# Kernel tuning notes

Hardware: AMD Instinct MI355X
Metric: run time of the kernel (lower is better)

The kernel has to match this reference:

```python
import jax, jax.numpy as jnp
import numpy as np

N_NODES = 50000
N_EDGES = 1600000
IN_DIM = 128
HEADS = 2
OUT_CH = 32
NEG_SLOPE = 0.2


def setup_inputs() -> dict:
    key = jax.random.key(0)
    k1, k2, k3, k4, k5, k6 = jax.random.split(key, 6)
    x = jax.random.normal(k1, (N_NODES, IN_DIM), dtype=jnp.float32)
    # Glorot-ish scale for weights
    W = jax.random.normal(k2, (IN_DIM, HEADS * OUT_CH), dtype=jnp.float32) * (1.0 / np.sqrt(IN_DIM))
    att_src = jax.random.normal(k3, (HEADS, OUT_CH), dtype=jnp.float32) * (1.0 / np.sqrt(OUT_CH))
    att_dst = jax.random.normal(k4, (HEADS, OUT_CH), dtype=jnp.float32) * (1.0 / np.sqrt(OUT_CH))
    bias = jnp.zeros((HEADS * OUT_CH,), dtype=jnp.float32)
    edge_index = jax.random.randint(k5, (2, N_EDGES), 0, N_NODES, dtype=jnp.int32)
    return {"x": x, "W": W, "att_src": att_src, "att_dst": att_dst,
            "bias": bias, "edge_index": edge_index}


def reference(x, W, att_src, att_dst, bias, edge_index):
    N = x.shape[0]
    # ELU on input features (IntraGraphAttention.forward)
    xf = jax.nn.elu(x)
    # Shared linear projection, per-head view: [N, H, C]
    h = (xf @ W).reshape(N, HEADS, OUT_CH)
    # add_self_loops=True (PyG GATConv default)
    loops = jnp.arange(N, dtype=edge_index.dtype)
    src = jnp.concatenate([edge_index[0], loops])
    dst = jnp.concatenate([edge_index[1], loops])
    # Per-node attention halves: [N, H]
    a_src = jnp.einsum('nhc,hc->nh', h, att_src)
    a_dst = jnp.einsum('nhc,hc->nh', h, att_dst)
    # Per-edge logits with leaky relu: [E, H]
    logits = a_src[src] + a_dst[dst]
    logits = jnp.where(logits >= 0, logits, NEG_SLOPE * logits)
    # Segment softmax over incoming edges of each dst node
    seg_max = jax.ops.segment_max(logits, dst, num_segments=N)
    e = jnp.exp(logits - seg_max[dst])
    denom = jax.ops.segment_sum(e, dst, num_segments=N)
    alpha = e / (denom[dst] + 1e-16)  # [E, H]
    # Weighted scatter-aggregate of source features: [N, H, C]
    msgs = h[src] * alpha[:, :, None]
    out = jax.ops.segment_sum(msgs, dst, num_segments=N)
    # concat=True -> [N, H*C], plus bias
    return out.reshape(N, HEADS * OUT_CH) + bias
```

## Files before the change

### kernel.cpp

```cpp
#include <hip/hip_runtime.h>
#include <hip/hip_bf16.h>

#define NN 50000
#define EE 1600000

using short8 = __attribute__((ext_vector_type(8))) short;
using float4v = __attribute__((ext_vector_type(4))) float;

__device__ __forceinline__ float bflo(unsigned u) { return __uint_as_float(u << 16); }
__device__ __forceinline__ float bfhi(unsigned u) { return __uint_as_float(u & 0xffff0000u); }
__device__ __forceinline__ unsigned short f2bf(float v) {
  return __bfloat16_as_ushort(__float2bfloat16(v));
}

__global__ __launch_bounds__(256) void k_pre(
    const float* __restrict__ x, const float* __restrict__ W,
    const float* __restrict__ att_src, const float* __restrict__ att_dst,
    float2* __restrict__ a_src2, float2* __restrict__ a_dst2,
    int* __restrict__ head8, int nblocks) {
  __shared__ float wa_s[128][2], wa_d[128][2];
  int tid = threadIdx.x;
  {
    int k = tid >> 1, hh = tid & 1;
    const float* wrow = W + k * 64 + hh * 32;
    const float* as = att_src + hh * 32;
    const float* ad = att_dst + hh * 32;
    float ss = 0.f, dd = 0.f;
#pragma unroll 8
    for (int c = 0; c < 32; ++c) { float wv = wrow[c]; ss += wv * as[c]; dd += wv * ad[c]; }
    wa_s[k][hh] = ss; wa_d[k][hh] = dd;
  }
  int gsize = nblocks * 256;
  for (int i = blockIdx.x * 256 + tid; i < NN * 8; i += gsize) head8[i] = -1;
  __syncthreads();
  int w = tid >> 6, lane = tid & 63;
  int nwaves = nblocks * 4;
  for (int n = blockIdx.x * 4 + w; n < NN; n += nwaves) {
    float x0 = x[n * 128 + lane], x1 = x[n * 128 + 64 + lane];
    x0 = x0 > 0.f ? x0 : __expf(x0) - 1.f;
    x1 = x1 > 0.f ? x1 : __expf(x1) - 1.f;
    float s0 = x0 * wa_s[lane][0] + x1 * wa_s[lane + 64][0];
    float s1 = x0 * wa_s[lane][1] + x1 * wa_s[lane + 64][1];
    float d0 = x0 * wa_d[lane][0] + x1 * wa_d[lane + 64][0];
    float d1 = x0 * wa_d[lane][1] + x1 * wa_d[lane + 64][1];
#pragma unroll
    for (int o = 32; o > 0; o >>= 1) {
      s0 += __shfl_xor(s0, o); s1 += __shfl_xor(s1, o);
      d0 += __shfl_xor(d0, o); d1 += __shfl_xor(d1, o);
    }
    if (lane == 0) { a_src2[n] = make_float2(s0, s1); a_dst2[n] = make_float2(d0, d1); }
  }
}

__global__ __launch_bounds__(256) void k_projm(
    const float* __restrict__ x, const float* __restrict__ W,
    unsigned* __restrict__ h2u) {
  __shared__ unsigned short Wt[64 * 136];
  __shared__ unsigned short xs[64 * 136];
  int tid = threadIdx.x;
  int row0 = blockIdx.x * 64;
  for (int i = tid; i < 8192; i += 256) {
    int k = i >> 6, n = i & 63;
    Wt[n * 136 + k] = f2bf(W[i]);
  }
  for (int i = tid; i < 4096; i += 256) {
    int r = i >> 6, k2 = (i & 63) * 2;
    int row = row0 + r;
    float v0 = 0.f, v1 = 0.f;
    if (row < NN) { float2 xv = *(const float2*)&x[row * 128 + k2]; v0 = xv.x; v1 = xv.y; }
    v0 = v0 > 0.f ? v0 : __expf(v0) - 1.f;
    v1 = v1 > 0.f ? v1 : __expf(v1) - 1.f;
    *(unsigned*)&xs[r * 136 + k2] = (unsigned)f2bf(v0) | ((unsigned)f2bf(v1) << 16);
  }
  __syncthreads();
  int w = tid >> 6, lane = tid & 63;
  int m = lane & 15, quad = lane >> 4;
  float4v acc[4] = {{0,0,0,0},{0,0,0,0},{0,0,0,0},{0,0,0,0}};
#pragma unroll
  for (int ks = 0; ks < 4; ++ks) {
    int koff = quad * 8 + ks * 32;
    short8 af = *(const short8*)&xs[(w * 16 + m) * 136 + koff];
#pragma unroll
    for (int nt = 0; nt < 4; ++nt) {
      short8 bf = *(const short8*)&Wt[(nt * 16 + m) * 136 + koff];
      acc[nt] = __builtin_amdgcn_mfma_f32_16x16x32_bf16(af, bf, acc[nt], 0, 0, 0);
    }
  }
#pragma unroll
  for (int nt = 0; nt < 4; ++nt) {
#pragma unroll
    for (int reg = 0; reg < 4; ++reg) {
      float v = acc[nt][reg];
      float vhi = __shfl_xor(v, 1);
      int row = row0 + w * 16 + quad * 4 + reg;
      if (!(m & 1) && row < NN) {
        h2u[row * 32 + nt * 8 + (m >> 1)] =
            (unsigned)f2bf(v) | ((unsigned)f2bf(vhi) << 16);
      }
    }
  }
}

__global__ __launch_bounds__(256) void k_build(
    const int* __restrict__ src, const int* __restrict__ dst,
    const float2* __restrict__ a_src2, const float2* __restrict__ a_dst2,
    int* __restrict__ head8, int4* __restrict__ edge4) {
  int e = blockIdx.x * 256 + threadIdx.x;
  int s = src[e], d = dst[e];
  float2 as = a_src2[s], ad = a_dst2[d];
  float l0 = as.x + ad.x; l0 = fmaxf(l0, 0.2f * l0);
  float l1 = as.y + ad.y; l1 = fmaxf(l1, 0.2f * l1);
  int old = atomicExch(&head8[d * 8 + (e & 7)], e);
  edge4[e] = make_int4(s, old, __float_as_int(__expf(l0)), __float_as_int(__expf(l1)));
}

__global__ __launch_bounds__(256) void k_agg(
    const unsigned* __restrict__ h2u, const float2* __restrict__ a_src2,
    const float2* __restrict__ a_dst2, const int4* __restrict__ head8v,
    const int4* __restrict__ edge4, const float* __restrict__ bias,
    float* __restrict__ out) {
  int n = blockIdx.x * 4 + (threadIdx.x >> 6);
  int lane = threadIdx.x & 63;
  int c2 = lane & 31;
  int half = lane >> 5;
  int hh = c2 >> 4;

  float denom = 0.f, acc0 = 0.f, acc1 = 0.f;
  if (half == 0) {
    float2 as = a_src2[n], ad = a_dst2[n];
    float l0 = (hh ? as.y + ad.y : as.x + ad.x);
    l0 = fmaxf(l0, 0.2f * l0);
    float es = __expf(l0);
    unsigned hv = h2u[n * 32 + c2];
    denom = es; acc0 = es * bflo(hv); acc1 = es * bfhi(hv);
  }

  int4 hd = head8v[n * 2 + half];
  int e0 = hd.x, e1 = hd.y, e2 = hd.z, e3 = hd.w;
  while (__any(max(max(e0, e1), max(e2, e3)) >= 0)) {
    int4 p0 = edge4[max(e0, 0)];
    int4 p1 = edge4[max(e1, 0)];
    int4 p2 = edge4[max(e2, 0)];
    int4 p3 = edge4[max(e3, 0)];
    unsigned h0 = h2u[p0.x * 32 + c2], h1 = h2u[p1.x * 32 + c2];
    unsigned h2 = h2u[p2.x * 32 + c2], h3 = h2u[p3.x * 32 + c2];
    float x0 = (e0 >= 0) ? __int_as_float(hh ? p0.w : p0.z) : 0.f;
    float x1 = (e1 >= 0) ? __int_as_float(hh ? p1.w : p1.z) : 0.f;
    float x2 = (e2 >= 0) ? __int_as_float(hh ? p2.w : p2.z) : 0.f;
    float x3 = (e3 >= 0) ? __int_as_float(hh ? p3.w : p3.z) : 0.f;
    denom += (x0 + x1) + (x2 + x3);
    acc0 += x0 * bflo(h0) + x1 * bflo(h1) + x2 * bflo(h2) + x3 * bflo(h3);
    acc1 += x0 * bfhi(h0) + x1 * bfhi(h1) + x2 * bfhi(h2) + x3 * bfhi(h3);
    e0 = (e0 >= 0) ? p0.y : -1;
    e1 = (e1 >= 0) ? p1.y : -1;
    e2 = (e2 >= 0) ? p2.y : -1;
    e3 = (e3 >= 0) ? p3.y : -1;
  }
  denom += __shfl_xor(denom, 32);
  acc0  += __shfl_xor(acc0, 32);
  acc1  += __shfl_xor(acc1, 32);
  if (half == 0) {
    float inv = 1.f / (denom + 1e-16f);
    float2 b = ((const float2*)bias)[c2];
    ((float2*)out)[n * 32 + c2] = make_float2(acc0 * inv + b.x, acc1 * inv + b.y);
  }
}

extern "C" void kernel_launch(void* const* d_in, const int* in_sizes, int n_in,
                              void* d_out, int out_size, void* d_ws, size_t ws_size,
                              hipStream_t stream) {
  const float* x       = (const float*)d_in[0];
  const float* W       = (const float*)d_in[1];
  const float* att_src = (const float*)d_in[2];
  const float* att_dst = (const float*)d_in[3];
  const float* bias    = (const float*)d_in[4];
  const int* edge_index = (const int*)d_in[5];
  const int* esrc = edge_index;
  const int* edst = edge_index + EE;

  char* base = (char*)d_ws;
  unsigned* h2u  = (unsigned*)base;
  float2* a_src2 = (float2*)(base + 6400000);
  float2* a_dst2 = (float2*)(base + 6800000);
  int*    head8  = (int*)(base + 7200000);
  int4*   edge4  = (int4*)(base + 8800000);

  const int PRE_BLOCKS = 1024;
  k_pre<<<PRE_BLOCKS, 256, 0, stream>>>(x, W, att_src, att_dst, a_src2, a_dst2,
                                        head8, PRE_BLOCKS);
  k_projm<<<(NN + 63) / 64, 256, 0, stream>>>(x, W, h2u);
  k_build<<<EE / 256, 256, 0, stream>>>(esrc, edst, a_src2, a_dst2, head8, edge4);
  k_agg<<<NN / 4, 256, 0, stream>>>(h2u, a_src2, a_dst2, (const int4*)head8,
                                    edge4, bias, (float*)d_out);
}
```

Baseline: 248.3 us.

## Fuse projection and edge-list build into one launch; use sentinel edge for list ends

Merges the MFMA projection kernel and the edge linked-list build kernel into a single launch, with block ID picking which role a block runs. Projection tiles shrink to 32 rows so there are more blocks and the two roles can overlap on the GPU. The aggregation loop now ends its lists on a sentinel edge record holding zero weights instead of -1, which removes the per-edge clamps and predicates. The cost is a bigger shared-memory footprint for edge-build blocks, which may lower their occupancy, and an extra workspace record at index EE.

```diff
diff --git a/kernel.cpp b/kernel.cpp
--- a/kernel.cpp
+++ b/kernel.cpp
@@ -3,6 +3,8 @@
 
 #define NN 50000
 #define EE 1600000
+#define SENT EE
+#define PROJ_BLOCKS 1563
 
 using short8 = __attribute__((ext_vector_type(8))) short;
 using float4v = __attribute__((ext_vector_type(4))) float;
@@ -17,7 +19,7 @@
     const float* __restrict__ x, const float* __restrict__ W,
     const float* __restrict__ att_src, const float* __restrict__ att_dst,
     float2* __restrict__ a_src2, float2* __restrict__ a_dst2,
-    int* __restrict__ head8, int nblocks) {
+    int* __restrict__ head8, int4* __restrict__ edge4, int nblocks) {
   __shared__ float wa_s[128][2], wa_d[128][2];
   int tid = threadIdx.x;
   {
@@ -31,7 +33,8 @@
     wa_s[k][hh] = ss; wa_d[k][hh] = dd;
   }
   int gsize = nblocks * 256;
-  for (int i = blockIdx.x * 256 + tid; i < NN * 8; i += gsize) head8[i] = -1;
+  for (int i = blockIdx.x * 256 + tid; i < NN * 8; i += gsize) head8[i] = SENT;
+  if (blockIdx.x == 0 && tid == 0) edge4[SENT] = make_int4(0, SENT, 0, 0);
   __syncthreads();
   int w = tid >> 6, lane = tid & 63;
   int nwaves = nblocks * 4;
@@ -52,18 +55,31 @@
   }
 }
 
-__global__ __launch_bounds__(256) void k_projm(
+__global__ __launch_bounds__(256) void k_mid(
     const float* __restrict__ x, const float* __restrict__ W,
-    unsigned* __restrict__ h2u) {
+    const int* __restrict__ src, const int* __restrict__ dst,
+    const float2* __restrict__ a_src2, const float2* __restrict__ a_dst2,
+    int* __restrict__ head8, int4* __restrict__ edge4, unsigned* __restrict__ h2u) {
+  int bid = blockIdx.x;
+  int tid = threadIdx.x;
+  if (bid >= PROJ_BLOCKS) {
+    int e = (bid - PROJ_BLOCKS) * 256 + tid;
+    int s = src[e], d = dst[e];
+    float2 as = a_src2[s], ad = a_dst2[d];
+    float l0 = as.x + ad.x; l0 = fmaxf(l0, 0.2f * l0);
+    float l1 = as.y + ad.y; l1 = fmaxf(l1, 0.2f * l1);
+    int old = atomicExch(&head8[d * 8 + (e & 7)], e);
+    edge4[e] = make_int4(s, old, __float_as_int(__expf(l0)), __float_as_int(__expf(l1)));
+    return;
+  }
   __shared__ unsigned short Wt[64 * 136];
-  __shared__ unsigned short xs[64 * 136];
-  int tid = threadIdx.x;
-  int row0 = blockIdx.x * 64;
+  __shared__ unsigned short xs[32 * 136];
+  int row0 = bid * 32;
   for (int i = tid; i < 8192; i += 256) {
     int k = i >> 6, n = i & 63;
     Wt[n * 136 + k] = f2bf(W[i]);
   }
-  for (int i = tid; i < 4096; i += 256) {
+  for (int i = tid; i < 2048; i += 256) {
     int r = i >> 6, k2 = (i & 63) * 2;
     int row = row0 + r;
     float v0 = 0.f, v1 = 0.f;
@@ -74,44 +90,34 @@
   }
   __syncthreads();
   int w = tid >> 6, lane = tid & 63;
+  int t = w >> 1, ch = w & 1;
   int m = lane & 15, quad = lane >> 4;
-  float4v acc[4] = {{0,0,0,0},{0,0,0,0},{0,0,0,0},{0,0,0,0}};
+  float4v acc[2] = {{0, 0, 0, 0}, {0, 0, 0, 0}};
 #pragma unroll
   for (int ks = 0; ks < 4; ++ks) {
     int koff = quad * 8 + ks * 32;
-    short8 af = *(const short8*)&xs[(w * 16 + m) * 136 + koff];
+    short8 af = *(const short8*)&xs[(t * 16 + m) * 136 + koff];
 #pragma unroll
-    for (int nt = 0; nt < 4; ++nt) {
+    for (int j = 0; j < 2; ++j) {
+      int nt = ch * 2 + j;
       short8 bf = *(const short8*)&Wt[(nt * 16 + m) * 136 + koff];
-      acc[nt] = __builtin_amdgcn_mfma_f32_16x16x32_bf16(af, bf, acc[nt], 0, 0, 0);
+      acc[j] = __builtin_amdgcn_mfma_f32_16x16x32_bf16(af, bf, acc[j], 0, 0, 0);
     }
   }
 #pragma unroll
-  for (int nt = 0; nt < 4; ++nt) {
+  for (int j = 0; j < 2; ++j) {
+    int nt = ch * 2 + j;
 #pragma unroll
     for (int reg = 0; reg < 4; ++reg) {
-      float v = acc[nt][reg];
+      float v = acc[j][reg];
       float vhi = __shfl_xor(v, 1);
-      int row = row0 + w * 16 + quad * 4 + reg;
+      int row = row0 + t * 16 + quad * 4 + reg;
       if (!(m & 1) && row < NN) {
         h2u[row * 32 + nt * 8 + (m >> 1)] =
             (unsigned)f2bf(v) | ((unsigned)f2bf(vhi) << 16);
       }
     }
   }
-}
-
-__global__ __launch_bounds__(256) void k_build(
-    const int* __restrict__ src, const int* __restrict__ dst,
-    const float2* __restrict__ a_src2, const float2* __restrict__ a_dst2,
-    int* __restrict__ head8, int4* __restrict__ edge4) {
-  int e = blockIdx.x * 256 + threadIdx.x;
-  int s = src[e], d = dst[e];
-  float2 as = a_src2[s], ad = a_dst2[d];
-  float l0 = as.x + ad.x; l0 = fmaxf(l0, 0.2f * l0);
-  float l1 = as.y + ad.y; l1 = fmaxf(l1, 0.2f * l1);
-  int old = atomicExch(&head8[d * 8 + (e & 7)], e);
-  edge4[e] = make_int4(s, old, __float_as_int(__expf(l0)), __float_as_int(__expf(l1)));
 }
 
 __global__ __launch_bounds__(256) void k_agg(
@@ -137,24 +143,21 @@
 
   int4 hd = head8v[n * 2 + half];
   int e0 = hd.x, e1 = hd.y, e2 = hd.z, e3 = hd.w;
-  while (__any(max(max(e0, e1), max(e2, e3)) >= 0)) {
-    int4 p0 = edge4[max(e0, 0)];
-    int4 p1 = edge4[max(e1, 0)];
-    int4 p2 = edge4[max(e2, 0)];
-    int4 p3 = edge4[max(e3, 0)];
+  while (__any(((e0 != SENT) | (e1 != SENT) | (e2 != SENT) | (e3 != SENT)) != 0)) {
+    int4 p0 = edge4[e0];
+    int4 p1 = edge4[e1];
+    int4 p2 = edge4[e2];
+    int4 p3 = edge4[e3];
     unsigned h0 = h2u[p0.x * 32 + c2], h1 = h2u[p1.x * 32 + c2];
     unsigned h2 = h2u[p2.x * 32 + c2], h3 = h2u[p3.x * 32 + c2];
-    float x0 = (e0 >= 0) ? __int_as_float(hh ? p0.w : p0.z) : 0.f;
-    float x1 = (e1 >= 0) ? __int_as_float(hh ? p1.w : p1.z) : 0.f;
-    float x2 = (e2 >= 0) ? __int_as_float(hh ? p2.w : p2.z) : 0.f;
-    float x3 = (e3 >= 0) ? __int_as_float(hh ? p3.w : p3.z) : 0.f;
+    float x0 = __int_as_float(hh ? p0.w : p0.z);
+    float x1 = __int_as_float(hh ? p1.w : p1.z);
+    float x2 = __int_as_float(hh ? p2.w : p2.z);
+    float x3 = __int_as_float(hh ? p3.w : p3.z);
     denom += (x0 + x1) + (x2 + x3);
     acc0 += x0 * bflo(h0) + x1 * bflo(h1) + x2 * bflo(h2) + x3 * bflo(h3);
     acc1 += x0 * bfhi(h0) + x1 * bfhi(h1) + x2 * bfhi(h2) + x3 * bfhi(h3);
-    e0 = (e0 >= 0) ? p0.y : -1;
-    e1 = (e1 >= 0) ? p1.y : -1;
-    e2 = (e2 >= 0) ? p2.y : -1;
-    e3 = (e3 >= 0) ? p3.y : -1;
+    e0 = p0.y; e1 = p1.y; e2 = p2.y; e3 = p3.y;
   }
   denom += __shfl_xor(denom, 32);
   acc0  += __shfl_xor(acc0, 32);
@@ -187,9 +190,9 @@
 
   const int PRE_BLOCKS = 1024;
   k_pre<<<PRE_BLOCKS, 256, 0, stream>>>(x, W, att_src, att_dst, a_src2, a_dst2,
-                                        head8, PRE_BLOCKS);
-  k_projm<<<(NN + 63) / 64, 256, 0, stream>>>(x, W, h2u);
-  k_build<<<EE / 256, 256, 0, stream>>>(esrc, edst, a_src2, a_dst2, head8, edge4);
+                                        head8, edge4, PRE_BLOCKS);
+  k_mid<<<PROJ_BLOCKS + EE / 256, 256, 0, stream>>>(x, W, esrc, edst, a_src2,
+                                                    a_dst2, head8, edge4, h2u);
   k_agg<<<NN / 4, 256, 0, stream>>>(h2u, a_src2, a_dst2, (const int4*)head8,
                                     edge4, bias, (float*)d_out);
 }
```

Result: slower. 258.5 us (+4.1%).
